# Kernel optimization log

Hardware: AMD Instinct MI355X
Metric: run time of the kernel (lower is better)

Reference implementation:

```python
import jax, jax.numpy as jnp
import numpy as np

NUM_GROUPS = 16
EPS = 1e-05
VARIANCE_FLOOR = 1e-06


def setup_inputs() -> dict:
    key = jax.random.key(0)
    k1, k2, k3, k4 = jax.random.split(key, 4)
    B, L, D, G = 4, 4096, 2048, NUM_GROUPS
    return {
        "x": jax.random.normal(k1, (B, L, D), dtype=jnp.float32),
        "prev_count": jnp.zeros((B,), dtype=jnp.int64 if jax.config.jax_enable_x64 else jnp.int32),
        "prev_mean": jax.random.normal(k2, (B, G), dtype=jnp.float32),
        "prev_var": jnp.ones((B, G), dtype=jnp.float32),
        "padding_mask": jnp.ones((B, L), dtype=bool),
        "weight": 0.1 * jax.random.normal(k3, (D,), dtype=jnp.float32),
        "bias": 0.1 * jax.random.normal(k4, (D,), dtype=jnp.float32),
    }


def reference(x, prev_count, prev_mean, prev_var, padding_mask, weight, bias):
    B, L, D = x.shape
    G = NUM_GROUPS
    gs = D // G
    x_groups = x.reshape(B, L, G, gs)                      # (B,L,G,gs)
    valid = padding_mask.astype(x.dtype)                   # (B,L)
    valid_exp = valid[..., None]                           # (B,L,1)

    group_means = x_groups.mean(axis=-1)                   # (B,L,G)
    prev_count_f = prev_count.astype(x.dtype)              # (B,)
    prev_sum = prev_mean * prev_count_f[:, None]           # (B,G)

    # streaming (cumsum-based Welford) mean
    cumsum_means = jnp.cumsum(group_means * valid_exp, axis=1)
    sum_t = prev_sum[:, None, :] + cumsum_means            # (B,L,G)
    count_t = prev_count_f[:, None] + jnp.cumsum(valid, axis=1)  # (B,L)
    count_clamped = jnp.maximum(count_t, 1.0)
    mean_t = jnp.where(count_t[..., None] > 0.0,
                       sum_t / count_clamped[..., None],
                       prev_mean[:, None, :])               # (B,L,G)

    # Welford M2 accumulation via prefix sums
    mean_prev = jnp.concatenate([prev_mean[:, None, :], mean_t[:, :-1, :]], axis=1)
    delta = group_means - mean_prev
    delta2 = group_means - mean_t
    prev_m2 = prev_var * jnp.maximum(prev_count_f, 1.0)[:, None]  # (B,G)
    m2_t = prev_m2[:, None, :] + jnp.cumsum(delta * delta2 * valid_exp, axis=1)
    var_t = jnp.where(count_t[..., None] > 0.0,
                      m2_t / count_clamped[..., None],
                      prev_var[:, None, :])
    var_t = jnp.maximum(var_t, VARIANCE_FLOOR)

    # normalize + affine
    x_hat = (x_groups - mean_t[..., None]) * jax.lax.rsqrt(var_t[..., None] + EPS)
    scale = (weight + 1.0).reshape(1, 1, G, gs)
    shift = bias.reshape(1, 1, G, gs)
    y = (x_hat * scale + shift).reshape(B, L, D)

    new_count = prev_count + padding_mask.astype(prev_count.dtype).sum(axis=1)
    return y, new_count, mean_t[:, -1, :], var_t[:, -1, :]
```

## Files before the change

### kernel.cpp

```cpp
#include <hip/hip_runtime.h>

#define NGROUPS 16
#define TPG     16
#define CHUNK   32
#define EPS_F   1e-5f
#define VFLOOR  1e-6f

__device__ __forceinline__ float sum8(const float4& a, const float4& b) {
    return ((a.x + a.y) + (a.z + a.w)) + ((b.x + b.y) + (b.z + b.w));
}

__device__ __forceinline__ void wmerge(float& na, float& ma, float& m2a,
                                       float nb, float mb, float m2b) {
    if (nb > 0.f) {
        float nn = na + nb;
        float d  = mb - ma;
        float r  = nb / nn;
        ma  = fmaf(d, r, ma);
        m2a = m2a + m2b + d * d * (na * r);
        na  = nn;
    }
}

__global__ void __launch_bounds__(256)
ts_gm_agg(const float* __restrict__ x, const int* __restrict__ mask,
          float* __restrict__ gm_buf, float4* __restrict__ loc4,
          int B, int L, int D, int NC, float inv_gs)
{
    const int b   = blockIdx.x / NC;
    const int c   = blockIdx.x % NC;
    const int tid = threadIdx.x;
    const int g   = tid / TPG;
    const bool leader = (tid & (TPG - 1)) == 0;
    const int t0  = c * CHUNK;
    const int t1  = min(t0 + CHUNK, L);

    const float* xb = x + (size_t)b * L * D + tid * 8;
    const int*   mb = mask + (size_t)b * L;
    float* gmo = gm_buf + (((size_t)b * NC + c) * NGROUPS + g) * CHUNK;

    float n = 0.f, mean = 0.f, m2 = 0.f;
    #pragma unroll 4
    for (int t = t0; t < t1; ++t) {
        const float4* p = (const float4*)(xb + (size_t)t * D);
        float4 v0 = p[0], v1 = p[1];
        float s = sum8(v0, v1);
        s += __shfl_xor(s, 1, 64);
        s += __shfl_xor(s, 2, 64);
        s += __shfl_xor(s, 4, 64);
        s += __shfl_xor(s, 8, 64);
        float gmv = s * inv_gs;
        if (leader) gmo[t - t0] = gmv;
        if (mb[t]) {
            n += 1.f;
            float d = gmv - mean;
            mean += __fdividef(d, n);
            m2 = fmaf(d, gmv - mean, m2);
        }
    }
    if (leader) {
        loc4[((size_t)b * NGROUPS + g) * NC + c] = make_float4(n, mean, m2, 0.f);
    }
}

__global__ void __launch_bounds__(256)
ts_fused(const float* __restrict__ x, const int* __restrict__ mask,
         const float* __restrict__ gm_buf, const float4* __restrict__ loc4,
         const int* __restrict__ prev_count, const float* __restrict__ prev_mean,
         const float* __restrict__ prev_var,
         const float* __restrict__ weight, const float* __restrict__ bias,
         float* __restrict__ y, float* __restrict__ out_count,
         float* __restrict__ out_mean, float* __restrict__ out_var,
         int B, int L, int D, int NC)
{
    __shared__ float s_mean[NGROUPS][CHUNK + 1];
    __shared__ float s_rstd[NGROUPS][CHUNK + 1];

    const int b   = blockIdx.x / NC;
    const int c   = blockIdx.x % NC;
    const int tid = threadIdx.x;
    const int g   = tid / TPG;
    const int k   = tid & (TPG - 1);
    const int chain = b * NGROUPS + g;

    float n = 0.f, mean = 0.f, m2 = 0.f;
    const float4* lrow = loc4 + (size_t)chain * NC;
    for (int cp = k; cp < c; cp += TPG) {
        float4 v = lrow[cp];
        wmerge(n, mean, m2, v.x, v.y, v.z);
    }
    #pragma unroll
    for (int o = 1; o < TPG; o <<= 1) {
        float on = __shfl_xor(n, o, 64);
        float om = __shfl_xor(mean, o, 64);
        float o2 = __shfl_xor(m2, o, 64);
        wmerge(n, mean, m2, on, om, o2);
    }
    {
        float pn = (float)prev_count[b];
        float pm = prev_mean[chain];
        float p2 = prev_var[chain] * fmaxf(pn, 1.0f);
        wmerge(pn, pm, p2, n, mean, m2);
        n = pn; mean = pm; m2 = p2;
    }

    const int t0 = c * CHUNK;
    const int jmax = min(CHUNK, L - t0);
    if (k == 0) {
        const float* gmo = gm_buf + (((size_t)b * NC + c) * NGROUPS + g) * CHUNK;
        const int*   mrow = mask + (size_t)b * L + t0;
        float var = fmaxf(__fdividef(m2, fmaxf(n, 1.f)), VFLOOR);
        #pragma unroll 8
        for (int j = 0; j < jmax; ++j) {
            float gmv = gmo[j];
            if (mrow[j]) {
                n += 1.f;
                float d = gmv - mean;
                mean += __fdividef(d, n);
                m2 = fmaf(d, gmv - mean, m2);
            }
            var = fmaxf(__fdividef(m2, fmaxf(n, 1.f)), VFLOOR);
            s_mean[g][j] = mean;
            s_rstd[g][j] = rsqrtf(var + EPS_F);
        }
        if (c == NC - 1) {
            out_mean[chain] = mean;
            out_var[chain]  = var;
            if (g == 0) out_count[b] = n;
        }
    }

    const float4* wp = (const float4*)(weight + tid * 8);
    const float4* hp = (const float4*)(bias + tid * 8);
    float4 w0 = wp[0], w1 = wp[1];
    float4 h0 = hp[0], h1 = hp[1];
    w0.x += 1.f; w0.y += 1.f; w0.z += 1.f; w0.w += 1.f;
    w1.x += 1.f; w1.y += 1.f; w1.z += 1.f; w1.w += 1.f;

    __syncthreads();

    const float* xb = x + ((size_t)b * L + t0) * D + tid * 8;
    float*       yb = y + ((size_t)b * L + t0) * D + tid * 8;
    #pragma unroll 2
    for (int j = 0; j < jmax; ++j) {
        float m_ = s_mean[g][j];
        float r_ = s_rstd[g][j];
        const float4* p = (const float4*)(xb + (size_t)j * D);
        float4 v0 = p[0], v1 = p[1];
        float4 o0, o1;
        o0.x = fmaf((v0.x - m_) * r_, w0.x, h0.x);
        o0.y = fmaf((v0.y - m_) * r_, w0.y, h0.y);
        o0.z = fmaf((v0.z - m_) * r_, w0.z, h0.z);
        o0.w = fmaf((v0.w - m_) * r_, w0.w, h0.w);
        o1.x = fmaf((v1.x - m_) * r_, w1.x, h1.x);
        o1.y = fmaf((v1.y - m_) * r_, w1.y, h1.y);
        o1.z = fmaf((v1.z - m_) * r_, w1.z, h1.z);
        o1.w = fmaf((v1.w - m_) * r_, w1.w, h1.w);
        float4* q = (float4*)(yb + (size_t)j * D);
        q[0] = o0; q[1] = o1;
    }
}

extern "C" void kernel_launch(void* const* d_in, const int* in_sizes, int n_in,
                              void* d_out, int out_size, void* d_ws, size_t ws_size,
                              hipStream_t stream) {
    const float* x          = (const float*)d_in[0];
    const int*   prev_count = (const int*)d_in[1];
    const float* prev_mean  = (const float*)d_in[2];
    const float* prev_var   = (const float*)d_in[3];
    const int*   mask       = (const int*)d_in[4];
    const float* weight     = (const float*)d_in[5];
    const float* bias       = (const float*)d_in[6];

    const int B  = in_sizes[1];
    const int D  = in_sizes[5];
    const int L  = in_sizes[4] / B;
    const int NC = (L + CHUNK - 1) / CHUNK;
    const int BG = B * NGROUPS;
    const float inv_gs = (float)NGROUPS / (float)D;

    float* out = (float*)d_out;
    const size_t yN = (size_t)B * L * D;
    float* out_y     = out;
    float* out_count = out + yN;
    float* out_mean  = out + yN + B;
    float* out_var   = out + yN + B + BG;

    float* ws = (float*)d_ws;
    const size_t gmN = (size_t)B * NC * NGROUPS * CHUNK;
    float*  gm_buf = ws;
    float4* loc4   = (float4*)(ws + gmN);

    dim3 blk(D / 8);

    ts_gm_agg<<<B * NC, blk, 0, stream>>>(x, mask, gm_buf, loc4, B, L, D, NC, inv_gs);

    ts_fused<<<B * NC, blk, 0, stream>>>(x, mask, gm_buf, loc4,
                                         prev_count, prev_mean, prev_var,
                                         weight, bias,
                                         out_y, out_count, out_mean, out_var,
                                         B, L, D, NC);
}
```

Measured before the change: 279.9 us.

## Fuse stats and normalize kernels into one cooperative kernel with grid sync

```diff
diff --git a/kernel.cpp b/kernel.cpp
--- a/kernel.cpp
+++ b/kernel.cpp
@@ -1,10 +1,15 @@
 #include <hip/hip_runtime.h>
+#include <hip/hip_cooperative_groups.h>
+
+namespace cg = cooperative_groups;
 
 #define NGROUPS 16
 #define TPG     16
 #define CHUNK   32
 #define EPS_F   1e-5f
 #define VFLOOR  1e-6f
+
+typedef float v4f __attribute__((ext_vector_type(4)));
 
 __device__ __forceinline__ float sum8(const float4& a, const float4& b) {
     return ((a.x + a.y) + (a.z + a.w)) + ((b.x + b.y) + (b.z + b.w));
@@ -22,22 +27,33 @@
     }
 }
 
-__global__ void __launch_bounds__(256)
-ts_gm_agg(const float* __restrict__ x, const int* __restrict__ mask,
-          float* __restrict__ gm_buf, float4* __restrict__ loc4,
-          int B, int L, int D, int NC, float inv_gs)
+__global__ void __launch_bounds__(256, 2)
+ts_coop(const float* __restrict__ x, const int* __restrict__ mask,
+        float4* __restrict__ loc4,
+        const int* __restrict__ prev_count, const float* __restrict__ prev_mean,
+        const float* __restrict__ prev_var,
+        const float* __restrict__ weight, const float* __restrict__ bias,
+        float* __restrict__ y, float* __restrict__ out_count,
+        float* __restrict__ out_mean, float* __restrict__ out_var,
+        int B, int L, int D, int NC, float inv_gs)
 {
+    __shared__ float s_gm[NGROUPS][CHUNK];
+    __shared__ float s_mean[NGROUPS][CHUNK + 1];
+    __shared__ float s_rstd[NGROUPS][CHUNK + 1];
+
     const int b   = blockIdx.x / NC;
     const int c   = blockIdx.x % NC;
     const int tid = threadIdx.x;
     const int g   = tid / TPG;
-    const bool leader = (tid & (TPG - 1)) == 0;
+    const int k   = tid & (TPG - 1);
+    const bool leader = (k == 0);
     const int t0  = c * CHUNK;
     const int t1  = min(t0 + CHUNK, L);
+    const int jmax = t1 - t0;
+    const int chain = b * NGROUPS + g;
 
     const float* xb = x + (size_t)b * L * D + tid * 8;
     const int*   mb = mask + (size_t)b * L;
-    float* gmo = gm_buf + (((size_t)b * NC + c) * NGROUPS + g) * CHUNK;
 
     float n = 0.f, mean = 0.f, m2 = 0.f;
     #pragma unroll 4
@@ -50,7 +66,7 @@
         s += __shfl_xor(s, 4, 64);
         s += __shfl_xor(s, 8, 64);
         float gmv = s * inv_gs;
-        if (leader) gmo[t - t0] = gmv;
+        if (leader) s_gm[g][t - t0] = gmv;
         if (mb[t]) {
             n += 1.f;
             float d = gmv - mean;
@@ -58,75 +74,57 @@
             m2 = fmaf(d, gmv - mean, m2);
         }
     }
+
     if (leader) {
-        loc4[((size_t)b * NGROUPS + g) * NC + c] = make_float4(n, mean, m2, 0.f);
-    }
-}
-
-__global__ void __launch_bounds__(256)
-ts_fused(const float* __restrict__ x, const int* __restrict__ mask,
-         const float* __restrict__ gm_buf, const float4* __restrict__ loc4,
-         const int* __restrict__ prev_count, const float* __restrict__ prev_mean,
-         const float* __restrict__ prev_var,
-         const float* __restrict__ weight, const float* __restrict__ bias,
-         float* __restrict__ y, float* __restrict__ out_count,
-         float* __restrict__ out_mean, float* __restrict__ out_var,
-         int B, int L, int D, int NC)
-{
-    __shared__ float s_mean[NGROUPS][CHUNK + 1];
-    __shared__ float s_rstd[NGROUPS][CHUNK + 1];
-
-    const int b   = blockIdx.x / NC;
-    const int c   = blockIdx.x % NC;
-    const int tid = threadIdx.x;
-    const int g   = tid / TPG;
-    const int k   = tid & (TPG - 1);
-    const int chain = b * NGROUPS + g;
-
-    float n = 0.f, mean = 0.f, m2 = 0.f;
-    const float4* lrow = loc4 + (size_t)chain * NC;
+        float* slot = (float*)&loc4[(size_t)(b * NC + c) * NGROUPS + g];
+        __hip_atomic_store(slot + 0, n,    __ATOMIC_RELAXED, __HIP_MEMORY_SCOPE_AGENT);
+        __hip_atomic_store(slot + 1, mean, __ATOMIC_RELAXED, __HIP_MEMORY_SCOPE_AGENT);
+        __hip_atomic_store(slot + 2, m2,   __ATOMIC_RELAXED, __HIP_MEMORY_SCOPE_AGENT);
+    }
+
+    cg::this_grid().sync();
+
+    float cn = 0.f, cm = 0.f, c2 = 0.f;
     for (int cp = k; cp < c; cp += TPG) {
-        float4 v = lrow[cp];
-        wmerge(n, mean, m2, v.x, v.y, v.z);
+        float* slot = (float*)&loc4[(size_t)(b * NC + cp) * NGROUPS + g];
+        float vn = __hip_atomic_load(slot + 0, __ATOMIC_RELAXED, __HIP_MEMORY_SCOPE_AGENT);
+        float vm = __hip_atomic_load(slot + 1, __ATOMIC_RELAXED, __HIP_MEMORY_SCOPE_AGENT);
+        float v2 = __hip_atomic_load(slot + 2, __ATOMIC_RELAXED, __HIP_MEMORY_SCOPE_AGENT);
+        wmerge(cn, cm, c2, vn, vm, v2);
     }
     #pragma unroll
     for (int o = 1; o < TPG; o <<= 1) {
-        float on = __shfl_xor(n, o, 64);
-        float om = __shfl_xor(mean, o, 64);
-        float o2 = __shfl_xor(m2, o, 64);
-        wmerge(n, mean, m2, on, om, o2);
-    }
-    {
-        float pn = (float)prev_count[b];
-        float pm = prev_mean[chain];
-        float p2 = prev_var[chain] * fmaxf(pn, 1.0f);
-        wmerge(pn, pm, p2, n, mean, m2);
-        n = pn; mean = pm; m2 = p2;
-    }
-
-    const int t0 = c * CHUNK;
-    const int jmax = min(CHUNK, L - t0);
-    if (k == 0) {
-        const float* gmo = gm_buf + (((size_t)b * NC + c) * NGROUPS + g) * CHUNK;
-        const int*   mrow = mask + (size_t)b * L + t0;
-        float var = fmaxf(__fdividef(m2, fmaxf(n, 1.f)), VFLOOR);
+        float on = __shfl_xor(cn, o, 64);
+        float om = __shfl_xor(cm, o, 64);
+        float o2 = __shfl_xor(c2, o, 64);
+        wmerge(cn, cm, c2, on, om, o2);
+    }
+    float pn = (float)prev_count[b];
+    float pm = prev_mean[chain];
+    float p2 = prev_var[chain] * fmaxf(pn, 1.0f);
+    wmerge(pn, pm, p2, cn, cm, c2);
+
+    if (leader) {
+        const int* mrow = mb + t0;
+        float rn = pn, rm = pm, r2 = p2;
+        float var = fmaxf(__fdividef(r2, fmaxf(rn, 1.f)), VFLOOR);
         #pragma unroll 8
         for (int j = 0; j < jmax; ++j) {
-            float gmv = gmo[j];
+            float gmv = s_gm[g][j];
             if (mrow[j]) {
-                n += 1.f;
-                float d = gmv - mean;
-                mean += __fdividef(d, n);
-                m2 = fmaf(d, gmv - mean, m2);
+                rn += 1.f;
+                float d = gmv - rm;
+                rm += __fdividef(d, rn);
+                r2 = fmaf(d, gmv - rm, r2);
             }
-            var = fmaxf(__fdividef(m2, fmaxf(n, 1.f)), VFLOOR);
-            s_mean[g][j] = mean;
+            var = fmaxf(__fdividef(r2, fmaxf(rn, 1.f)), VFLOOR);
+            s_mean[g][j] = rm;
             s_rstd[g][j] = rsqrtf(var + EPS_F);
         }
         if (c == NC - 1) {
-            out_mean[chain] = mean;
+            out_mean[chain] = rm;
             out_var[chain]  = var;
-            if (g == 0) out_count[b] = n;
+            if (g == 0) out_count[b] = rn;
         }
     }
 
@@ -139,15 +137,15 @@
 
     __syncthreads();
 
-    const float* xb = x + ((size_t)b * L + t0) * D + tid * 8;
+    const float* xr = x + ((size_t)b * L + t0) * D + tid * 8;
     float*       yb = y + ((size_t)b * L + t0) * D + tid * 8;
     #pragma unroll 2
     for (int j = 0; j < jmax; ++j) {
         float m_ = s_mean[g][j];
         float r_ = s_rstd[g][j];
-        const float4* p = (const float4*)(xb + (size_t)j * D);
+        const float4* p = (const float4*)(xr + (size_t)j * D);
         float4 v0 = p[0], v1 = p[1];
-        float4 o0, o1;
+        v4f o0, o1;
         o0.x = fmaf((v0.x - m_) * r_, w0.x, h0.x);
         o0.y = fmaf((v0.y - m_) * r_, w0.y, h0.y);
         o0.z = fmaf((v0.z - m_) * r_, w0.z, h0.z);
@@ -156,8 +154,9 @@
         o1.y = fmaf((v1.y - m_) * r_, w1.y, h1.y);
         o1.z = fmaf((v1.z - m_) * r_, w1.z, h1.z);
         o1.w = fmaf((v1.w - m_) * r_, w1.w, h1.w);
-        float4* q = (float4*)(yb + (size_t)j * D);
-        q[0] = o0; q[1] = o1;
+        v4f* q = (v4f*)(yb + (size_t)j * D);
+        __builtin_nontemporal_store(o0, q);
+        __builtin_nontemporal_store(o1, q + 1);
     }
 }
 
@@ -186,18 +185,17 @@
     float* out_mean  = out + yN + B;
     float* out_var   = out + yN + B + BG;
 
-    float* ws = (float*)d_ws;
-    const size_t gmN = (size_t)B * NC * NGROUPS * CHUNK;
-    float*  gm_buf = ws;
-    float4* loc4   = (float4*)(ws + gmN);
-
-    dim3 blk(D / 8);
-
-    ts_gm_agg<<<B * NC, blk, 0, stream>>>(x, mask, gm_buf, loc4, B, L, D, NC, inv_gs);
-
-    ts_fused<<<B * NC, blk, 0, stream>>>(x, mask, gm_buf, loc4,
-                                         prev_count, prev_mean, prev_var,
-                                         weight, bias,
-                                         out_y, out_count, out_mean, out_var,
-                                         B, L, D, NC);
-}
+    float4* loc4 = (float4*)d_ws;
+
+    void* args[] = {
+        (void*)&x, (void*)&mask, (void*)&loc4,
+        (void*)&prev_count, (void*)&prev_mean, (void*)&prev_var,
+        (void*)&weight, (void*)&bias,
+        (void*)&out_y, (void*)&out_count, (void*)&out_mean, (void*)&out_var,
+        (void*)&B, (void*)&L, (void*)&D, (void*)&NC, (void*)&inv_gs
+    };
+
+    (void)hipLaunchCooperativeKernel((const void*)ts_coop,
+                                     dim3(B * NC), dim3(D / 8),
+                                     args, 0, stream);
+}
```

Result: slower. 361.1 us (+29.0%).
